# Kernel tuning notes

Hardware: AMD Instinct MI355X
Metric: run time of the kernel (lower is better)

## Reference

```python
import jax, jax.numpy as jnp
import numpy as np

S1, S2, B, H, E, IN, OUT, NL = 8, 32, 256, 1024, 512, 2, 2, 4


def setup_inputs() -> dict:
    key = jax.random.key(0)
    ks = jax.random.split(key, 20)
    s_h = 1.0 / np.sqrt(H)
    inp = {
        'input': jax.random.normal(ks[0], (B, IN), jnp.float32),
        'h0': jax.random.normal(ks[1], (NL, B, H), jnp.float32) * 0.5,
        'c0': jax.random.normal(ks[2], (NL, B, H), jnp.float32) * 0.5,
        'all_outputs': jax.random.normal(ks[3], (S1, S2, B, H), jnp.float32),
        'W_emb': jax.random.normal(ks[4], (E, IN), jnp.float32) / np.sqrt(IN),
        'b_emb': jax.random.normal(ks[5], (E,), jnp.float32) * 0.01,
        'W_attn': jax.random.normal(ks[6], (1, 2 * H), jnp.float32) / np.sqrt(2 * H),
        'b_attn': jax.random.normal(ks[7], (1,), jnp.float32) * 0.01,
        'Wih0': jax.random.normal(ks[8], (4 * H, E + H), jnp.float32) / np.sqrt(E + H),
        'Whh0': jax.random.normal(ks[9], (4 * H, H), jnp.float32) * s_h,
        'bih0': jax.random.normal(ks[10], (4 * H,), jnp.float32) * 0.01,
        'bhh0': jax.random.normal(ks[11], (4 * H,), jnp.float32) * 0.01,
        'Wih_r': jax.random.normal(ks[12], (NL - 1, 4 * H, H), jnp.float32) * s_h,
        'Whh_r': jax.random.normal(ks[13], (NL - 1, 4 * H, H), jnp.float32) * s_h,
        'bih_r': jax.random.normal(ks[14], (NL - 1, 4 * H), jnp.float32) * 0.01,
        'bhh_r': jax.random.normal(ks[15], (NL - 1, 4 * H), jnp.float32) * 0.01,
        'W_out': jax.random.normal(ks[16], (OUT, H), jnp.float32) * s_h,
        'b_out': jax.random.normal(ks[17], (OUT,), jnp.float32) * 0.01,
    }
    return inp


def _lstm_cell(x, h, c, Wih, Whh, bih, bhh):
    g = x @ Wih.T + h @ Whh.T + bih + bhh  # [B, 4H], torch gate order i,f,g,o
    i, f, gg, o = jnp.split(g, 4, axis=1)
    c2 = jax.nn.sigmoid(f) * c + jax.nn.sigmoid(i) * jnp.tanh(gg)
    h2 = jax.nn.sigmoid(o) * jnp.tanh(c2)
    return h2, c2


def reference(input, h0, c0, all_outputs, W_emb, b_emb, W_attn, b_attn,
              Wih0, Whh0, bih0, bhh0, Wih_r, Whh_r, bih_r, bhh_r, W_out, b_out):
    s1, s2, b, h_dim = all_outputs.shape
    # embedding (dropout = identity in eval mode)
    embedded = jax.nn.relu(input @ W_emb.T + b_emb)  # [B, E]
    h_top = h0[0]  # [B, H]
    # attn(cat(h_top, y)) decomposed: h part is shared across all (j, i)
    w_h = W_attn[0, :h_dim]
    w_y = W_attn[0, h_dim:]
    scores = (jnp.einsum('jibh,h->jib', all_outputs, w_y)
              + (h_top @ w_h)[None, None, :] + b_attn[0])  # [S1, S2, B]
    # torch cats per-(j,i) [B,1] columns j-major -> [B, S1*S2]
    normalized = jax.nn.softmax(scores.reshape(s1 * s2, b).T, axis=1)  # [B, S1*S2]
    temp = normalized.reshape(b, s1, s2)
    # NOTE: original writes into an expand()-ed zero buffer, so every j-slice
    # aliases the same memory; after the loop all slices equal the last j's bmm
    # result and sum(0) multiplies it by S1. We replicate that exactly.
    applied_last = jnp.einsum('bi,ibh->bh', temp[:, -1, :], all_outputs[-1])  # [B, H]
    final_attn = s1 * applied_last
    x = jnp.concatenate([final_attn, embedded], axis=1)  # [B, H+E]
    hs, cs = [], []
    h, c = _lstm_cell(x, h0[0], c0[0], Wih0, Whh0, bih0, bhh0)
    hs.append(h); cs.append(c)
    for l in range(Wih_r.shape[0]):  # inter-layer dropout = identity in eval
        h, c = _lstm_cell(h, h0[l + 1], c0[l + 1], Wih_r[l], Whh_r[l], bih_r[l], bhh_r[l])
        hs.append(h); cs.append(c)
    h_new = jnp.stack(hs)
    c_new = jnp.stack(cs)
    final_output = h @ W_out.T + b_out  # [B, OUT]
    return final_output, h_new, c_new, normalized
```

## Files before the change

### kernel.cpp

```cpp
#include <hip/hip_runtime.h>
#include <hip/hip_bf16.h>

typedef __bf16 bf16x8 __attribute__((ext_vector_type(8)));
typedef float  f32x4  __attribute__((ext_vector_type(4)));

#define O_FINAL 0
#define O_H     512
#define O_C     1049088
#define O_NORM  2097664

__device__ __forceinline__ bf16x8 cvt8(float4 a, float4 b) {
  bf16x8 r;
  r[0] = (__bf16)a.x; r[1] = (__bf16)a.y; r[2] = (__bf16)a.z; r[3] = (__bf16)a.w;
  r[4] = (__bf16)b.x; r[5] = (__bf16)b.y; r[6] = (__bf16)b.z; r[7] = (__bf16)b.w;
  return r;
}

template<int K>
__device__ __forceinline__ void tile_gemm_ff(const float* __restrict__ A,
                                             const float* __restrict__ W,
                                             int r0, int j0, char* lds,
                                             f32x4 acc[2]) {
  constexpr int NK = K / 64;
  constexpr int D = 4;
  const int t = threadIdx.x, lane = t & 63, wave = t >> 6;
  const int rf = wave & 3, gg = wave >> 2;
  const int tr = t >> 3, chunk = t & 7;
  const float* wsrc = W + (size_t)((tr >> 4) * 1024 + j0 + (tr & 15)) * K + chunk * 8;
  const float* asrc = A + (size_t)(r0 + tr) * K + chunk * 8;
  const int sw_off = (chunk ^ (tr & 7)) << 4;
  const int woff = 8192 + tr * 128 + sw_off;
  const int aoff = tr * 128 + sw_off;
  const int a_tr  = rf * 16 + (lane & 15);
  const int w_tr0 = gg * 32 + (lane & 15);
  const int w_tr1 = w_tr0 + 16;
  const int ksel  = lane >> 4;

  float4 wp[D][2], ap[D][2];
#pragma unroll
  for (int d = 0; d < D; ++d) {
    wp[d][0] = *(const float4*)(wsrc + d * 64);
    wp[d][1] = *(const float4*)(wsrc + d * 64 + 4);
    ap[d][0] = *(const float4*)(asrc + d * 64);
    ap[d][1] = *(const float4*)(asrc + d * 64 + 4);
  }
#pragma unroll
  for (int s = 0; s < NK; ++s) {
    const int sl = s % D;
    char* buf = lds + (s & 1) * 16384;
    *(bf16x8*)(buf + aoff) = cvt8(ap[sl][0], ap[sl][1]);
    *(bf16x8*)(buf + woff) = cvt8(wp[sl][0], wp[sl][1]);
    if (s + D < NK) {
      wp[sl][0] = *(const float4*)(wsrc + (s + D) * 64);
      wp[sl][1] = *(const float4*)(wsrc + (s + D) * 64 + 4);
      ap[sl][0] = *(const float4*)(asrc + (s + D) * 64);
      ap[sl][1] = *(const float4*)(asrc + (s + D) * 64 + 4);
    }
    __syncthreads();
#pragma unroll
    for (int s2 = 0; s2 < 2; ++s2) {
      const int chk = s2 * 4 + ksel;
      bf16x8 af  = *(const bf16x8*)(buf + a_tr * 128 + ((chk ^ (a_tr & 7)) << 4));
      bf16x8 wf0 = *(const bf16x8*)(buf + 8192 + w_tr0 * 128 + ((chk ^ (w_tr0 & 7)) << 4));
      bf16x8 wf1 = *(const bf16x8*)(buf + 8192 + w_tr1 * 128 + ((chk ^ (w_tr1 & 7)) << 4));
      acc[0] = __builtin_amdgcn_mfma_f32_16x16x32_bf16(af, wf0, acc[0], 0, 0, 0);
      acc[1] = __builtin_amdgcn_mfma_f32_16x16x32_bf16(af, wf1, acc[1], 0, 0, 0);
    }
  }
}

__global__ __launch_bounds__(256) void k_scores(const float* __restrict__ AO,
                                                const float* __restrict__ Wattn,
                                                float* __restrict__ sc) {
  const int lane = threadIdx.x & 63, wave = threadIdx.x >> 6;
  const float* wy = Wattn + 1024;
  float4 wv[4];
#pragma unroll
  for (int q = 0; q < 4; ++q) wv[q] = *(const float4*)(wy + lane * 4 + 256 * q);
  const int row0 = (blockIdx.x * 4 + wave) * 4;
  float a4[4];
#pragma unroll
  for (int rr = 0; rr < 4; ++rr) {
    const float4* rp = (const float4*)(AO + (size_t)(row0 + rr) * 1024);
    float a = 0.f;
#pragma unroll
    for (int q = 0; q < 4; ++q) {
      float4 v = rp[lane + 64 * q];
      a += v.x * wv[q].x + v.y * wv[q].y + v.z * wv[q].z + v.w * wv[q].w;
    }
    a4[rr] = a;
  }
#pragma unroll
  for (int rr = 0; rr < 4; ++rr) {
    float a = a4[rr];
#pragma unroll
    for (int off = 32; off; off >>= 1) a += __shfl_xor(a, off, 64);
    if (lane == 0) {
      int row = row0 + rr;
      sc[(row & 255) * 256 + (row >> 8)] = a;
    }
  }
}

__global__ __launch_bounds__(512) void k_mid(
    const float* __restrict__ sc,   const float* __restrict__ AO,
    const float* __restrict__ inp,  const float* __restrict__ Wemb,
    const float* __restrict__ bemb,
    const float* __restrict__ h0,
    const float* __restrict__ Whh0, const float* __restrict__ Whh_r,
    const float* __restrict__ bih0, const float* __restrict__ bhh0,
    const float* __restrict__ bih_r, const float* __restrict__ bhh_r,
    float* __restrict__ Gh,
    float* __restrict__ norm_out,   __bf16* __restrict__ xb) {
  __shared__ char smem[32768];
  const int t = threadIdx.x, lane = t & 63, wave = t >> 6;
  if (blockIdx.x < 1024) {
    const int j = blockIdx.x;
    const int l = j >> 8, inner = j & 255;
    const int cb = inner & 63, rb = inner >> 6;
    const int j0 = cb * 16, r0 = rb * 64;
    const float* A  = h0 + (size_t)l * 262144;
    const float* W  = (l == 0) ? Whh0 : (Whh_r + (size_t)(l - 1) * 4194304);
    const float* bi = (l == 0) ? bih0 : (bih_r + (size_t)(l - 1) * 4096);
    const float* bh = (l == 0) ? bhh0 : (bhh_r + (size_t)(l - 1) * 4096);
    f32x4 acc[2] = {};
    tile_gemm_ff<1024>(A, W, r0, j0, smem, acc);
    float* Go = Gh + (size_t)l * 1048576;
    const int rf = wave & 3, gg = wave >> 2;
    const int col = j0 + (lane & 15);
    const int rbase = r0 + rf * 16 + ((lane >> 4) << 2);
#pragma unroll
    for (int gi = 0; gi < 2; ++gi) {
      const int cg = (gg * 2 + gi) * 1024 + col;
#pragma unroll
      for (int q = 0; q < 4; ++q)
        Go[(size_t)(rbase + q) * 4096 + cg] = acc[gi][q] + bi[cg] + bh[cg];
    }
    return;
  }
  float* red  = (float*)smem;
  float* nv_l = (float*)(smem + 64);
  const int b = blockIdx.x - 1024;
  float s = (t < 256) ? sc[b * 256 + t] : -3.4e38f;
  float m = s;
#pragma unroll
  for (int off = 32; off; off >>= 1) m = fmaxf(m, __shfl_xor(m, off, 64));
  if (lane == 0) red[wave] = m;
  __syncthreads();
  m = red[0];
#pragma unroll
  for (int w2 = 1; w2 < 8; ++w2) m = fmaxf(m, red[w2]);
  float e = (t < 256) ? __expf(s - m) : 0.f;
  float sum = e;
#pragma unroll
  for (int off = 32; off; off >>= 1) sum += __shfl_xor(sum, off, 64);
  __syncthreads();
  if (lane == 0) red[wave] = sum;
  __syncthreads();
  sum = red[0];
#pragma unroll
  for (int w2 = 1; w2 < 8; ++w2) sum += red[w2];
  float nv = e / sum;
  if (t < 256) {
    norm_out[b * 256 + t] = nv;
    if (t >= 224) nv_l[t - 224] = nv;
  }
  __syncthreads();
  float a0 = 0.f, a1 = 0.f;
  const float* base = AO + ((size_t)224 * 256 + b) * 1024;
#pragma unroll 4
  for (int i = 0; i < 32; ++i) {
    float w = nv_l[i];
    const float* rp = base + (size_t)i * 262144;
    a0 += w * rp[t];
    a1 += w * rp[t + 512];
  }
  xb[(size_t)b * 1536 + t]       = (__bf16)(8.0f * a0);
  xb[(size_t)b * 1536 + t + 512] = (__bf16)(8.0f * a1);
  float e2 = inp[b * 2] * Wemb[t * 2] + inp[b * 2 + 1] * Wemb[t * 2 + 1] + bemb[t];
  xb[(size_t)b * 1536 + 1024 + t] = (__bf16)fmaxf(e2, 0.f);
}

template<int KA>
__global__ __launch_bounds__(512) void k_layer(const __bf16* __restrict__ A,
                                               const float* __restrict__ Wih,
                                               const float* __restrict__ Gh,
                                               const float* __restrict__ c0l,
                                               float* __restrict__ h_out,
                                               float* __restrict__ c_out,
                                               __bf16* __restrict__ hb) {
  __shared__ char smem[40960];
  float* exch = (float*)(smem + 32768);
  const int t = threadIdx.x, lane = t & 63, wave = t >> 6;
  const int rf = wave & 3, gg = wave >> 2;
  const int cb = blockIdx.x & 63, rb = blockIdx.x >> 6;
  const int j0 = cb * 16, r0 = rb * 64;
  {
    constexpr int NK = KA / 64;
    constexpr int D = 4;
    const int tr = t >> 3, chunk = t & 7;
    const float*  wsrc = Wih + (size_t)((tr >> 4) * 1024 + j0 + (tr & 15)) * KA + chunk * 8;
    const __bf16* asrc = A + (size_t)(r0 + tr) * KA + chunk * 8;
    const int sw_off = (chunk ^ (tr & 7)) << 4;
    const int woff = 8192 + tr * 128 + sw_off;
    const int aoff = tr * 128 + sw_off;
    const int a_tr  = rf * 16 + (lane & 15);
    const int w_tr0 = gg * 32 + (lane & 15);
    const int w_tr1 = w_tr0 + 16;
    const int ksel  = lane >> 4;
    f32x4 acc[2] = {};
    float4 wp[D][2]; bf16x8 ap[D];
#pragma unroll
    for (int d = 0; d < D; ++d) {
      wp[d][0] = *(const float4*)(wsrc + d * 64);
      wp[d][1] = *(const float4*)(wsrc + d * 64 + 4);
      ap[d]    = *(const bf16x8*)(asrc + d * 64);
    }
#pragma unroll
    for (int s = 0; s < NK; ++s) {
      const int sl = s % D;
      char* buf = smem + (s & 1) * 16384;
      *(bf16x8*)(buf + aoff) = ap[sl];
      *(bf16x8*)(buf + woff) = cvt8(wp[sl][0], wp[sl][1]);
      if (s + D < NK) {
        wp[sl][0] = *(const float4*)(wsrc + (s + D) * 64);
        wp[sl][1] = *(const float4*)(wsrc + (s + D) * 64 + 4);
        ap[sl]    = *(const bf16x8*)(asrc + (s + D) * 64);
      }
      __syncthreads();
#pragma unroll
      for (int s2 = 0; s2 < 2; ++s2) {
        const int chk = s2 * 4 + ksel;
        bf16x8 af  = *(const bf16x8*)(buf + a_tr * 128 + ((chk ^ (a_tr & 7)) << 4));
        bf16x8 wf0 = *(const bf16x8*)(buf + 8192 + w_tr0 * 128 + ((chk ^ (w_tr0 & 7)) << 4));
        bf16x8 wf1 = *(const bf16x8*)(buf + 8192 + w_tr1 * 128 + ((chk ^ (w_tr1 & 7)) << 4));
        acc[0] = __builtin_amdgcn_mfma_f32_16x16x32_bf16(af, wf0, acc[0], 0, 0, 0);
        acc[1] = __builtin_amdgcn_mfma_f32_16x16x32_bf16(af, wf1, acc[1], 0, 0, 0);
      }
    }
    const int col = j0 + (lane & 15);
    const int rbase = r0 + rf * 16 + ((lane >> 4) << 2);
    const int eidx = ((lane >> 4) << 2) * 16 + (lane & 15);
#pragma unroll
    for (int gi = 0; gi < 2; ++gi) {
      const float* gp = Gh + (size_t)rbase * 4096 + (gg * 2 + gi) * 1024 + col;
#pragma unroll
      for (int q = 0; q < 4; ++q) acc[gi][q] += gp[(size_t)q * 4096];
    }
    __syncthreads();
    if (gg == 1) {
#pragma unroll
      for (int gi = 0; gi < 2; ++gi)
#pragma unroll
        for (int q = 0; q < 4; ++q)
          exch[(rf * 2 + gi) * 256 + eidx + q * 16] = acc[gi][q];
    }
    __syncthreads();
    if (gg == 0) {
#pragma unroll
      for (int q = 0; q < 4; ++q) {
        const int row = rbase + q;
        float gv = exch[(rf * 2 + 0) * 256 + eidx + q * 16];
        float ov = exch[(rf * 2 + 1) * 256 + eidx + q * 16];
        float si = 1.f / (1.f + __expf(-acc[0][q]));
        float sf = 1.f / (1.f + __expf(-acc[1][q]));
        float so = 1.f / (1.f + __expf(-ov));
        float c2 = sf * c0l[(size_t)row * 1024 + col] + si * tanhf(gv);
        float h2 = so * tanhf(c2);
        h_out[(size_t)row * 1024 + col] = h2;
        c_out[(size_t)row * 1024 + col] = c2;
        hb[(size_t)row * 1024 + col] = (__bf16)h2;
      }
    }
  }
}

__global__ __launch_bounds__(256) void k_final(const float* __restrict__ h3,
                                               const float* __restrict__ Wout,
                                               const float* __restrict__ bout,
                                               float* __restrict__ out) {
  const int lane = threadIdx.x & 63, wave = threadIdx.x >> 6;
  const int b = blockIdx.x * 4 + wave;
  const float4* hp = (const float4*)(h3 + (size_t)b * 1024);
  const float4* w0 = (const float4*)Wout;
  const float4* w1 = (const float4*)(Wout + 1024);
  float a0 = 0.f, a1 = 0.f;
#pragma unroll
  for (int q = 0; q < 4; ++q) {
    float4 hv = hp[lane + 64 * q];
    float4 v0 = w0[lane + 64 * q];
    float4 v1 = w1[lane + 64 * q];
    a0 += hv.x * v0.x + hv.y * v0.y + hv.z * v0.z + hv.w * v0.w;
    a1 += hv.x * v1.x + hv.y * v1.y + hv.z * v1.z + hv.w * v1.w;
  }
#pragma unroll
  for (int off = 32; off; off >>= 1) {
    a0 += __shfl_xor(a0, off, 64);
    a1 += __shfl_xor(a1, off, 64);
  }
  if (lane == 0) {
    out[b * 2]     = a0 + bout[0];
    out[b * 2 + 1] = a1 + bout[1];
  }
}

extern "C" void kernel_launch(void* const* d_in, const int* in_sizes, int n_in,
                              void* d_out, int out_size, void* d_ws, size_t ws_size,
                              hipStream_t stream) {
  const float* inp    = (const float*)d_in[0];
  const float* h0     = (const float*)d_in[1];
  const float* c0     = (const float*)d_in[2];
  const float* AO     = (const float*)d_in[3];
  const float* Wemb   = (const float*)d_in[4];
  const float* bemb   = (const float*)d_in[5];
  const float* Wattn  = (const float*)d_in[6];
  const float* Wih0   = (const float*)d_in[8];
  const float* Whh0   = (const float*)d_in[9];
  const float* bih0   = (const float*)d_in[10];
  const float* bhh0   = (const float*)d_in[11];
  const float* Wih_r  = (const float*)d_in[12];
  const float* Whh_r  = (const float*)d_in[13];
  const float* bih_r  = (const float*)d_in[14];
  const float* bhh_r  = (const float*)d_in[15];
  const float* Wout   = (const float*)d_in[16];
  const float* bout   = (const float*)d_in[17];

  float* out = (float*)d_out;
  char* ws = (char*)d_ws;

  float*  sc = (float*)ws;
  float*  Gh = (float*)(ws + 262144);
  __bf16* xb = (__bf16*)(ws + 17039360);
  __bf16* hb = (__bf16*)(ws + 17825792);

  k_scores<<<4096, 256, 0, stream>>>(AO, Wattn, sc);
  k_mid<<<1280, 512, 0, stream>>>(sc, AO, inp, Wemb, bemb, h0, Whh0, Whh_r,
                                  bih0, bhh0, bih_r, bhh_r, Gh,
                                  out + O_NORM, xb);

  k_layer<1536><<<256, 512, 0, stream>>>(xb, Wih0, Gh, c0,
                                         out + O_H, out + O_C, hb);
  for (int l = 1; l < 4; ++l)
    k_layer<1024><<<256, 512, 0, stream>>>(hb + (size_t)(l - 1) * 262144,
                                           Wih_r + (size_t)(l - 1) * 4194304,
                                           Gh + (size_t)l * 1048576,
                                           c0 + (size_t)l * 262144,
                                           out + O_H + (size_t)l * 262144,
                                           out + O_C + (size_t)l * 262144,
                                           hb + (size_t)l * 262144);

  k_final<<<64, 256, 0, stream>>>(out + O_H + 3 * 262144, Wout, bout, out + O_FINAL);
}
```

Measured before the change: 152.3 us.

## Halve per-block column tile in LSTM layer kernel to double grid size

Each layer block now covers 8 hidden columns (32 gate rows) instead of 16, so the launch goes from 256 to 512 blocks. The aim is to fill more of the GPU's compute units in a launch-bound, weight-streaming GEMM. Each wave now does one MFMA per k-step. The gate exchange is reworked to pair i/f through a cross-lane shuffle and g/o through LDS. The cost is that the A tile is loaded twice as often across blocks, and the smaller tile gives more LDS overhead per MFMA.

```diff
diff --git a/kernel.cpp b/kernel.cpp
--- a/kernel.cpp
+++ b/kernel.cpp
@@ -2,6 +2,7 @@
 #include <hip/hip_bf16.h>
 
 typedef __bf16 bf16x8 __attribute__((ext_vector_type(8)));
+typedef __bf16 bf16x4 __attribute__((ext_vector_type(4)));
 typedef float  f32x4  __attribute__((ext_vector_type(4)));
 
 #define O_FINAL 0
@@ -13,6 +14,11 @@
   bf16x8 r;
   r[0] = (__bf16)a.x; r[1] = (__bf16)a.y; r[2] = (__bf16)a.z; r[3] = (__bf16)a.w;
   r[4] = (__bf16)b.x; r[5] = (__bf16)b.y; r[6] = (__bf16)b.z; r[7] = (__bf16)b.w;
+  return r;
+}
+__device__ __forceinline__ bf16x4 cvt4(float4 a) {
+  bf16x4 r;
+  r[0] = (__bf16)a.x; r[1] = (__bf16)a.y; r[2] = (__bf16)a.z; r[3] = (__bf16)a.w;
   return r;
 }
 
@@ -189,81 +195,74 @@
                                                float* __restrict__ h_out,
                                                float* __restrict__ c_out,
                                                __bf16* __restrict__ hb) {
-  __shared__ char smem[40960];
-  float* exch = (float*)(smem + 32768);
+  constexpr int NK = KA / 64;
+  constexpr int D = 4;
+  __shared__ char smem[28672];
+  float* exch = (float*)(smem + 24576);
   const int t = threadIdx.x, lane = t & 63, wave = t >> 6;
-  const int rf = wave & 3, gg = wave >> 2;
-  const int cb = blockIdx.x & 63, rb = blockIdx.x >> 6;
-  const int j0 = cb * 16, r0 = rb * 64;
-  {
-    constexpr int NK = KA / 64;
-    constexpr int D = 4;
-    const int tr = t >> 3, chunk = t & 7;
-    const float*  wsrc = Wih + (size_t)((tr >> 4) * 1024 + j0 + (tr & 15)) * KA + chunk * 8;
-    const __bf16* asrc = A + (size_t)(r0 + tr) * KA + chunk * 8;
-    const int sw_off = (chunk ^ (tr & 7)) << 4;
-    const int woff = 8192 + tr * 128 + sw_off;
-    const int aoff = tr * 128 + sw_off;
-    const int a_tr  = rf * 16 + (lane & 15);
-    const int w_tr0 = gg * 32 + (lane & 15);
-    const int w_tr1 = w_tr0 + 16;
-    const int ksel  = lane >> 4;
-    f32x4 acc[2] = {};
-    float4 wp[D][2]; bf16x8 ap[D];
-#pragma unroll
-    for (int d = 0; d < D; ++d) {
-      wp[d][0] = *(const float4*)(wsrc + d * 64);
-      wp[d][1] = *(const float4*)(wsrc + d * 64 + 4);
-      ap[d]    = *(const bf16x8*)(asrc + d * 64);
-    }
-#pragma unroll
-    for (int s = 0; s < NK; ++s) {
-      const int sl = s % D;
-      char* buf = smem + (s & 1) * 16384;
-      *(bf16x8*)(buf + aoff) = ap[sl];
-      *(bf16x8*)(buf + woff) = cvt8(wp[sl][0], wp[sl][1]);
-      if (s + D < NK) {
-        wp[sl][0] = *(const float4*)(wsrc + (s + D) * 64);
-        wp[sl][1] = *(const float4*)(wsrc + (s + D) * 64 + 4);
-        ap[sl]    = *(const bf16x8*)(asrc + (s + D) * 64);
-      }
-      __syncthreads();
-#pragma unroll
-      for (int s2 = 0; s2 < 2; ++s2) {
-        const int chk = s2 * 4 + ksel;
-        bf16x8 af  = *(const bf16x8*)(buf + a_tr * 128 + ((chk ^ (a_tr & 7)) << 4));
-        bf16x8 wf0 = *(const bf16x8*)(buf + 8192 + w_tr0 * 128 + ((chk ^ (w_tr0 & 7)) << 4));
-        bf16x8 wf1 = *(const bf16x8*)(buf + 8192 + w_tr1 * 128 + ((chk ^ (w_tr1 & 7)) << 4));
-        acc[0] = __builtin_amdgcn_mfma_f32_16x16x32_bf16(af, wf0, acc[0], 0, 0, 0);
-        acc[1] = __builtin_amdgcn_mfma_f32_16x16x32_bf16(af, wf1, acc[1], 0, 0, 0);
-      }
-    }
-    const int col = j0 + (lane & 15);
-    const int rbase = r0 + rf * 16 + ((lane >> 4) << 2);
-    const int eidx = ((lane >> 4) << 2) * 16 + (lane & 15);
-#pragma unroll
-    for (int gi = 0; gi < 2; ++gi) {
-      const float* gp = Gh + (size_t)rbase * 4096 + (gg * 2 + gi) * 1024 + col;
-#pragma unroll
-      for (int q = 0; q < 4; ++q) acc[gi][q] += gp[(size_t)q * 4096];
+  const int rf = wave & 3, cf = wave >> 2;
+  const int cb = blockIdx.x & 127, rb = blockIdx.x >> 7;
+  const int j0 = cb * 8, r0 = rb * 64;
+  const int wr = t >> 4, wch = t & 15;
+  const float* wsrc = Wih + (size_t)((wr >> 3) * 1024 + j0 + (wr & 7)) * KA + wch * 4;
+  const int woff = 8192 + wr * 128 + ((((wch >> 1) ^ (wr & 7)) << 4) | ((wch & 1) << 3));
+  const int atr = t >> 3, ach = t & 7;
+  const __bf16* asrc = A + (size_t)(r0 + atr) * KA + ach * 8;
+  const int aoff = atr * 128 + ((ach ^ (atr & 7)) << 4);
+  const int a_tr = rf * 16 + (lane & 15);
+  const int w_tr = cf * 16 + (lane & 15);
+  const int ksel = lane >> 4;
+
+  float4 wp[D]; bf16x8 ap[D];
+#pragma unroll
+  for (int d = 0; d < D; ++d) {
+    wp[d] = *(const float4*)(wsrc + d * 64);
+    ap[d] = *(const bf16x8*)(asrc + d * 64);
+  }
+  f32x4 acc = {0.f, 0.f, 0.f, 0.f};
+#pragma unroll
+  for (int s = 0; s < NK; ++s) {
+    const int sl = s % D;
+    char* buf = smem + (s & 1) * 12288;
+    *(bf16x8*)(buf + aoff) = ap[sl];
+    *(bf16x4*)(buf + woff) = cvt4(wp[sl]);
+    if (s + D < NK) {
+      wp[sl] = *(const float4*)(wsrc + (s + D) * 64);
+      ap[sl] = *(const bf16x8*)(asrc + (s + D) * 64);
     }
     __syncthreads();
-    if (gg == 1) {
-#pragma unroll
-      for (int gi = 0; gi < 2; ++gi)
-#pragma unroll
-        for (int q = 0; q < 4; ++q)
-          exch[(rf * 2 + gi) * 256 + eidx + q * 16] = acc[gi][q];
-    }
-    __syncthreads();
-    if (gg == 0) {
+#pragma unroll
+    for (int s2 = 0; s2 < 2; ++s2) {
+      const int chk = s2 * 4 + ksel;
+      bf16x8 af = *(const bf16x8*)(buf + a_tr * 128 + ((chk ^ (a_tr & 7)) << 4));
+      bf16x8 wf = *(const bf16x8*)(buf + 8192 + w_tr * 128 + ((chk ^ (w_tr & 7)) << 4));
+      acc = __builtin_amdgcn_mfma_f32_16x16x32_bf16(af, wf, acc, 0, 0, 0);
+    }
+  }
+  const int gate = cf * 2 + ((lane & 15) >> 3);
+  const int col  = j0 + (lane & 7);
+  const int rbase = r0 + rf * 16 + ((lane >> 4) << 2);
+#pragma unroll
+  for (int q = 0; q < 4; ++q)
+    acc[q] += Gh[(size_t)(rbase + q) * 4096 + gate * 1024 + col];
+  if (cf == 1) {
+#pragma unroll
+    for (int q = 0; q < 4; ++q)
+      exch[(rf * 64 + lane) * 4 + q] = acc[q];
+  }
+  __syncthreads();
+  if (cf == 0) {
+    float fv[4];
+#pragma unroll
+    for (int q = 0; q < 4; ++q) fv[q] = __shfl_xor(acc[q], 8, 64);
+    if ((lane & 8) == 0) {
 #pragma unroll
       for (int q = 0; q < 4; ++q) {
         const int row = rbase + q;
-        float gv = exch[(rf * 2 + 0) * 256 + eidx + q * 16];
-        float ov = exch[(rf * 2 + 1) * 256 + eidx + q * 16];
-        float si = 1.f / (1.f + __expf(-acc[0][q]));
-        float sf = 1.f / (1.f + __expf(-acc[1][q]));
+        float gv = exch[(rf * 64 + lane) * 4 + q];
+        float ov = exch[(rf * 64 + (lane | 8)) * 4 + q];
+        float si = 1.f / (1.f + __expf(-acc[q]));
+        float sf = 1.f / (1.f + __expf(-fv[q]));
         float so = 1.f / (1.f + __expf(-ov));
         float c2 = sf * c0l[(size_t)row * 1024 + col] + si * tanhf(gv);
         float h2 = so * tanhf(c2);
@@ -338,10 +337,10 @@
                                   bih0, bhh0, bih_r, bhh_r, Gh,
                                   out + O_NORM, xb);
 
-  k_layer<1536><<<256, 512, 0, stream>>>(xb, Wih0, Gh, c0,
+  k_layer<1536><<<512, 512, 0, stream>>>(xb, Wih0, Gh, c0,
                                          out + O_H, out + O_C, hb);
   for (int l = 1; l < 4; ++l)
-    k_layer<1024><<<256, 512, 0, stream>>>(hb + (size_t)(l - 1) * 262144,
+    k_layer<1024><<<512, 512, 0, stream>>>(hb + (size_t)(l - 1) * 262144,
                                            Wih_r + (size_t)(l - 1) * 4194304,
                                            Gh + (size_t)l * 1048576,
                                            c0 + (size_t)l * 262144,
```

Result: slower. 164.2 us (+7.9%).

## Fuse LSTM layers and output projection into persistent kernel with grid barriers

Applied to the files above, without the earlier changes.

Replaces the four per-layer launches and the final projection launch with a single persistent 256-block kernel. Layers are separated by atomic-counter grid barriers, and the barrier counters are cleared with a memset on every call. The new kernel also recomputes the softmax-normalised attention and embedding input, even though the middle kernel is still launched and already produces them. The goal is to remove inter-kernel launch gaps. The cost is barrier spin-waits, duplicated attention work that re-reads a large slice of all_outputs, and reliance on all 256 blocks being resident at once.

```diff
diff --git a/kernel.cpp b/kernel.cpp
--- a/kernel.cpp
+++ b/kernel.cpp
@@ -4,10 +4,22 @@
 typedef __bf16 bf16x8 __attribute__((ext_vector_type(8)));
 typedef float  f32x4  __attribute__((ext_vector_type(4)));
 
+#define GRID2 256
 #define O_FINAL 0
 #define O_H     512
 #define O_C     1049088
 #define O_NORM  2097664
+
+__device__ __forceinline__ void gridbar(int* slot) {
+  __syncthreads();
+  if (threadIdx.x == 0) {
+    __hip_atomic_fetch_add(slot, 1, __ATOMIC_ACQ_REL, __HIP_MEMORY_SCOPE_AGENT);
+    while (__hip_atomic_load(slot, __ATOMIC_RELAXED, __HIP_MEMORY_SCOPE_AGENT) < GRID2)
+      __builtin_amdgcn_s_sleep(2);
+    (void)__hip_atomic_load(slot, __ATOMIC_ACQUIRE, __HIP_MEMORY_SCOPE_AGENT);
+  }
+  __syncthreads();
+}
 
 __device__ __forceinline__ bf16x8 cvt8(float4 a, float4 b) {
   bf16x8 r;
@@ -182,125 +194,192 @@
 }
 
 template<int KA>
-__global__ __launch_bounds__(512) void k_layer(const __bf16* __restrict__ A,
-                                               const float* __restrict__ Wih,
-                                               const float* __restrict__ Gh,
-                                               const float* __restrict__ c0l,
-                                               float* __restrict__ h_out,
-                                               float* __restrict__ c_out,
-                                               __bf16* __restrict__ hb) {
-  __shared__ char smem[40960];
+__device__ __forceinline__ void layer_body(const __bf16* __restrict__ A,
+                                           const float* __restrict__ Wih,
+                                           const float* __restrict__ Gh,
+                                           const float* __restrict__ c0l,
+                                           float* __restrict__ h_out,
+                                           float* __restrict__ c_out,
+                                           __bf16* __restrict__ hb,
+                                           char* smem) {
+  constexpr int NK = KA / 64;
+  constexpr int D = 4;
   float* exch = (float*)(smem + 32768);
   const int t = threadIdx.x, lane = t & 63, wave = t >> 6;
   const int rf = wave & 3, gg = wave >> 2;
   const int cb = blockIdx.x & 63, rb = blockIdx.x >> 6;
   const int j0 = cb * 16, r0 = rb * 64;
+  const int tr = t >> 3, chunk = t & 7;
+  const float*  wsrc = Wih + (size_t)((tr >> 4) * 1024 + j0 + (tr & 15)) * KA + chunk * 8;
+  const __bf16* asrc = A + (size_t)(r0 + tr) * KA + chunk * 8;
+  const int sw_off = (chunk ^ (tr & 7)) << 4;
+  const int woff = 8192 + tr * 128 + sw_off;
+  const int aoff = tr * 128 + sw_off;
+  const int a_tr  = rf * 16 + (lane & 15);
+  const int w_tr0 = gg * 32 + (lane & 15);
+  const int w_tr1 = w_tr0 + 16;
+  const int ksel  = lane >> 4;
+  f32x4 acc[2] = {};
+  float4 wp[D][2]; bf16x8 ap[D];
+#pragma unroll
+  for (int d = 0; d < D; ++d) {
+    wp[d][0] = *(const float4*)(wsrc + d * 64);
+    wp[d][1] = *(const float4*)(wsrc + d * 64 + 4);
+    ap[d]    = *(const bf16x8*)(asrc + d * 64);
+  }
+#pragma unroll
+  for (int s = 0; s < NK; ++s) {
+    const int sl = s % D;
+    char* buf = smem + (s & 1) * 16384;
+    *(bf16x8*)(buf + aoff) = ap[sl];
+    *(bf16x8*)(buf + woff) = cvt8(wp[sl][0], wp[sl][1]);
+    if (s + D < NK) {
+      wp[sl][0] = *(const float4*)(wsrc + (s + D) * 64);
+      wp[sl][1] = *(const float4*)(wsrc + (s + D) * 64 + 4);
+      ap[sl]    = *(const bf16x8*)(asrc + (s + D) * 64);
+    }
+    __syncthreads();
+#pragma unroll
+    for (int s2 = 0; s2 < 2; ++s2) {
+      const int chk = s2 * 4 + ksel;
+      bf16x8 af  = *(const bf16x8*)(buf + a_tr * 128 + ((chk ^ (a_tr & 7)) << 4));
+      bf16x8 wf0 = *(const bf16x8*)(buf + 8192 + w_tr0 * 128 + ((chk ^ (w_tr0 & 7)) << 4));
+      bf16x8 wf1 = *(const bf16x8*)(buf + 8192 + w_tr1 * 128 + ((chk ^ (w_tr1 & 7)) << 4));
+      acc[0] = __builtin_amdgcn_mfma_f32_16x16x32_bf16(af, wf0, acc[0], 0, 0, 0);
+      acc[1] = __builtin_amdgcn_mfma_f32_16x16x32_bf16(af, wf1, acc[1], 0, 0, 0);
+    }
+  }
+  const int col = j0 + (lane & 15);
+  const int rbase = r0 + rf * 16 + ((lane >> 4) << 2);
+  const int eidx = ((lane >> 4) << 2) * 16 + (lane & 15);
+#pragma unroll
+  for (int gi = 0; gi < 2; ++gi) {
+    const float* gp = Gh + (size_t)rbase * 4096 + (gg * 2 + gi) * 1024 + col;
+#pragma unroll
+    for (int q = 0; q < 4; ++q) acc[gi][q] += gp[(size_t)q * 4096];
+  }
+  __syncthreads();
+  if (gg == 1) {
+#pragma unroll
+    for (int gi = 0; gi < 2; ++gi)
+#pragma unroll
+      for (int q = 0; q < 4; ++q)
+        exch[(rf * 2 + gi) * 256 + eidx + q * 16] = acc[gi][q];
+  }
+  __syncthreads();
+  if (gg == 0) {
+#pragma unroll
+    for (int q = 0; q < 4; ++q) {
+      const int row = rbase + q;
+      float gv = exch[(rf * 2 + 0) * 256 + eidx + q * 16];
+      float ov = exch[(rf * 2 + 1) * 256 + eidx + q * 16];
+      float si = 1.f / (1.f + __expf(-acc[0][q]));
+      float sf = 1.f / (1.f + __expf(-acc[1][q]));
+      float so = 1.f / (1.f + __expf(-ov));
+      float c2 = sf * c0l[(size_t)row * 1024 + col] + si * tanhf(gv);
+      float h2 = so * tanhf(c2);
+      h_out[(size_t)row * 1024 + col] = h2;
+      c_out[(size_t)row * 1024 + col] = c2;
+      hb[(size_t)row * 1024 + col] = (__bf16)h2;
+    }
+  }
+}
+
+__global__ __launch_bounds__(512) void k_tail(
+    const float* __restrict__ sc,   const float* __restrict__ AO,
+    const float* __restrict__ inp,  const float* __restrict__ Wemb,
+    const float* __restrict__ bemb,
+    const float* __restrict__ Wih0, const float* __restrict__ Wih_r,
+    const float* __restrict__ Gh,   const float* __restrict__ c0,
+    const float* __restrict__ Wout, const float* __restrict__ bout,
+    float* __restrict__ out, int* __restrict__ bar,
+    __bf16* __restrict__ xb, __bf16* __restrict__ hb) {
+  __shared__ char smem[40960];
+  const int t = threadIdx.x, lane = t & 63, wave = t >> 6;
+
   {
-    constexpr int NK = KA / 64;
-    constexpr int D = 4;
-    const int tr = t >> 3, chunk = t & 7;
-    const float*  wsrc = Wih + (size_t)((tr >> 4) * 1024 + j0 + (tr & 15)) * KA + chunk * 8;
-    const __bf16* asrc = A + (size_t)(r0 + tr) * KA + chunk * 8;
-    const int sw_off = (chunk ^ (tr & 7)) << 4;
-    const int woff = 8192 + tr * 128 + sw_off;
-    const int aoff = tr * 128 + sw_off;
-    const int a_tr  = rf * 16 + (lane & 15);
-    const int w_tr0 = gg * 32 + (lane & 15);
-    const int w_tr1 = w_tr0 + 16;
-    const int ksel  = lane >> 4;
-    f32x4 acc[2] = {};
-    float4 wp[D][2]; bf16x8 ap[D];
-#pragma unroll
-    for (int d = 0; d < D; ++d) {
-      wp[d][0] = *(const float4*)(wsrc + d * 64);
-      wp[d][1] = *(const float4*)(wsrc + d * 64 + 4);
-      ap[d]    = *(const bf16x8*)(asrc + d * 64);
-    }
-#pragma unroll
-    for (int s = 0; s < NK; ++s) {
-      const int sl = s % D;
-      char* buf = smem + (s & 1) * 16384;
-      *(bf16x8*)(buf + aoff) = ap[sl];
-      *(bf16x8*)(buf + woff) = cvt8(wp[sl][0], wp[sl][1]);
-      if (s + D < NK) {
-        wp[sl][0] = *(const float4*)(wsrc + (s + D) * 64);
-        wp[sl][1] = *(const float4*)(wsrc + (s + D) * 64 + 4);
-        ap[sl]    = *(const bf16x8*)(asrc + (s + D) * 64);
-      }
-      __syncthreads();
-#pragma unroll
-      for (int s2 = 0; s2 < 2; ++s2) {
-        const int chk = s2 * 4 + ksel;
-        bf16x8 af  = *(const bf16x8*)(buf + a_tr * 128 + ((chk ^ (a_tr & 7)) << 4));
-        bf16x8 wf0 = *(const bf16x8*)(buf + 8192 + w_tr0 * 128 + ((chk ^ (w_tr0 & 7)) << 4));
-        bf16x8 wf1 = *(const bf16x8*)(buf + 8192 + w_tr1 * 128 + ((chk ^ (w_tr1 & 7)) << 4));
-        acc[0] = __builtin_amdgcn_mfma_f32_16x16x32_bf16(af, wf0, acc[0], 0, 0, 0);
-        acc[1] = __builtin_amdgcn_mfma_f32_16x16x32_bf16(af, wf1, acc[1], 0, 0, 0);
-      }
-    }
-    const int col = j0 + (lane & 15);
-    const int rbase = r0 + rf * 16 + ((lane >> 4) << 2);
-    const int eidx = ((lane >> 4) << 2) * 16 + (lane & 15);
-#pragma unroll
-    for (int gi = 0; gi < 2; ++gi) {
-      const float* gp = Gh + (size_t)rbase * 4096 + (gg * 2 + gi) * 1024 + col;
-#pragma unroll
-      for (int q = 0; q < 4; ++q) acc[gi][q] += gp[(size_t)q * 4096];
-    }
-    __syncthreads();
-    if (gg == 1) {
-#pragma unroll
-      for (int gi = 0; gi < 2; ++gi)
-#pragma unroll
-        for (int q = 0; q < 4; ++q)
-          exch[(rf * 2 + gi) * 256 + eidx + q * 16] = acc[gi][q];
-    }
-    __syncthreads();
-    if (gg == 0) {
-#pragma unroll
-      for (int q = 0; q < 4; ++q) {
-        const int row = rbase + q;
-        float gv = exch[(rf * 2 + 0) * 256 + eidx + q * 16];
-        float ov = exch[(rf * 2 + 1) * 256 + eidx + q * 16];
-        float si = 1.f / (1.f + __expf(-acc[0][q]));
-        float sf = 1.f / (1.f + __expf(-acc[1][q]));
-        float so = 1.f / (1.f + __expf(-ov));
-        float c2 = sf * c0l[(size_t)row * 1024 + col] + si * tanhf(gv);
-        float h2 = so * tanhf(c2);
-        h_out[(size_t)row * 1024 + col] = h2;
-        c_out[(size_t)row * 1024 + col] = c2;
-        hb[(size_t)row * 1024 + col] = (__bf16)h2;
-      }
-    }
-  }
-}
-
-__global__ __launch_bounds__(256) void k_final(const float* __restrict__ h3,
-                                               const float* __restrict__ Wout,
-                                               const float* __restrict__ bout,
-                                               float* __restrict__ out) {
-  const int lane = threadIdx.x & 63, wave = threadIdx.x >> 6;
-  const int b = blockIdx.x * 4 + wave;
-  const float4* hp = (const float4*)(h3 + (size_t)b * 1024);
-  const float4* w0 = (const float4*)Wout;
-  const float4* w1 = (const float4*)(Wout + 1024);
-  float a0 = 0.f, a1 = 0.f;
-#pragma unroll
-  for (int q = 0; q < 4; ++q) {
-    float4 hv = hp[lane + 64 * q];
-    float4 v0 = w0[lane + 64 * q];
-    float4 v1 = w1[lane + 64 * q];
-    a0 += hv.x * v0.x + hv.y * v0.y + hv.z * v0.z + hv.w * v0.w;
-    a1 += hv.x * v1.x + hv.y * v1.y + hv.z * v1.z + hv.w * v1.w;
-  }
-#pragma unroll
-  for (int off = 32; off; off >>= 1) {
-    a0 += __shfl_xor(a0, off, 64);
-    a1 += __shfl_xor(a1, off, 64);
-  }
-  if (lane == 0) {
-    out[b * 2]     = a0 + bout[0];
-    out[b * 2 + 1] = a1 + bout[1];
+    float* red  = (float*)smem;
+    float* nv_l = (float*)(smem + 64);
+    const int b = blockIdx.x;
+    float s = (t < 256) ? sc[b * 256 + t] : -3.4e38f;
+    float m = s;
+#pragma unroll
+    for (int off = 32; off; off >>= 1) m = fmaxf(m, __shfl_xor(m, off, 64));
+    if (lane == 0) red[wave] = m;
+    __syncthreads();
+    m = red[0];
+#pragma unroll
+    for (int w2 = 1; w2 < 8; ++w2) m = fmaxf(m, red[w2]);
+    float e = (t < 256) ? __expf(s - m) : 0.f;
+    float sum = e;
+#pragma unroll
+    for (int off = 32; off; off >>= 1) sum += __shfl_xor(sum, off, 64);
+    __syncthreads();
+    if (lane == 0) red[wave] = sum;
+    __syncthreads();
+    sum = red[0];
+#pragma unroll
+    for (int w2 = 1; w2 < 8; ++w2) sum += red[w2];
+    float nv = e / sum;
+    if (t < 256) {
+      out[O_NORM + b * 256 + t] = nv;
+      if (t >= 224) nv_l[t - 224] = nv;
+    }
+    __syncthreads();
+    float a0 = 0.f, a1 = 0.f;
+    const float* base = AO + ((size_t)224 * 256 + b) * 1024;
+#pragma unroll 4
+    for (int i = 0; i < 32; ++i) {
+      float w = nv_l[i];
+      const float* rp = base + (size_t)i * 262144;
+      a0 += w * rp[t];
+      a1 += w * rp[t + 512];
+    }
+    xb[(size_t)b * 1536 + t]       = (__bf16)(8.0f * a0);
+    xb[(size_t)b * 1536 + t + 512] = (__bf16)(8.0f * a1);
+    float e2 = inp[b * 2] * Wemb[t * 2] + inp[b * 2 + 1] * Wemb[t * 2 + 1] + bemb[t];
+    xb[(size_t)b * 1536 + 1024 + t] = (__bf16)fmaxf(e2, 0.f);
+  }
+  gridbar(bar + 0 * 32);
+
+  layer_body<1536>(xb, Wih0, Gh, c0, out + O_H, out + O_C, hb, smem);
+  gridbar(bar + 1 * 32);
+#pragma unroll 1
+  for (int l = 1; l < 4; ++l) {
+    layer_body<1024>(hb + (size_t)(l - 1) * 262144,
+                     Wih_r + (size_t)(l - 1) * 4194304,
+                     Gh + (size_t)l * 1048576,
+                     c0 + (size_t)l * 262144,
+                     out + O_H + (size_t)l * 262144,
+                     out + O_C + (size_t)l * 262144,
+                     hb + (size_t)l * 262144, smem);
+    gridbar(bar + (l + 1) * 32);
+  }
+
+  if (blockIdx.x < 32) {
+    const float* h3 = out + O_H + 3 * 262144;
+    const int bb = blockIdx.x * 8 + wave;
+    const float4* hp = (const float4*)(h3 + (size_t)bb * 1024);
+    const float4* w0 = (const float4*)Wout;
+    const float4* w1 = (const float4*)(Wout + 1024);
+    float a0 = 0.f, a1 = 0.f;
+#pragma unroll
+    for (int q = 0; q < 4; ++q) {
+      float4 hv = hp[lane + 64 * q];
+      float4 v0 = w0[lane + 64 * q];
+      float4 v1 = w1[lane + 64 * q];
+      a0 += hv.x * v0.x + hv.y * v0.y + hv.z * v0.z + hv.w * v0.w;
+      a1 += hv.x * v1.x + hv.y * v1.y + hv.z * v1.z + hv.w * v1.w;
+    }
+#pragma unroll
+    for (int off = 32; off; off >>= 1) {
+      a0 += __shfl_xor(a0, off, 64);
+      a1 += __shfl_xor(a1, off, 64);
+    }
+    if (lane == 0) {
+      out[bb * 2]     = a0 + bout[0];
+      out[bb * 2 + 1] = a1 + bout[1];
+    }
   }
 }
 
@@ -328,26 +407,17 @@
   float* out = (float*)d_out;
   char* ws = (char*)d_ws;
 
-  float*  sc = (float*)ws;
-  float*  Gh = (float*)(ws + 262144);
-  __bf16* xb = (__bf16*)(ws + 17039360);
-  __bf16* hb = (__bf16*)(ws + 17825792);
-
+  int*    bar = (int*)ws;
+  float*  sc  = (float*)(ws + 4096);
+  float*  Gh  = (float*)(ws + 266240);
+  __bf16* xb  = (__bf16*)(ws + 17043456);
+  __bf16* hb  = (__bf16*)(ws + 17829888);
+
+  hipMemsetAsync(bar, 0, 4096, stream);
   k_scores<<<4096, 256, 0, stream>>>(AO, Wattn, sc);
   k_mid<<<1280, 512, 0, stream>>>(sc, AO, inp, Wemb, bemb, h0, Whh0, Whh_r,
                                   bih0, bhh0, bih_r, bhh_r, Gh,
                                   out + O_NORM, xb);
-
-  k_layer<1536><<<256, 512, 0, stream>>>(xb, Wih0, Gh, c0,
-                                         out + O_H, out + O_C, hb);
-  for (int l = 1; l < 4; ++l)
-    k_layer<1024><<<256, 512, 0, stream>>>(hb + (size_t)(l - 1) * 262144,
-                                           Wih_r + (size_t)(l - 1) * 4194304,
-                                           Gh + (size_t)l * 1048576,
-                                           c0 + (size_t)l * 262144,
-                                           out + O_H + (size_t)l * 262144,
-                                           out + O_C + (size_t)l * 262144,
-                                           hb + (size_t)l * 262144);
-
-  k_final<<<64, 256, 0, stream>>>(out + O_H + 3 * 262144, Wout, bout, out + O_FINAL);
-}
+  k_tail<<<256, 512, 0, stream>>>(sc, AO, inp, Wemb, bemb, Wih0, Wih_r,
+                                  Gh, c0, Wout, bout, out, bar, xb, hb);
+}
```

Measured after the change: 255.3 us. 67.6% more time.
